# Performance work log

Hardware: AMD Instinct MI355X
Metric: run time of the kernel (lower is better)

Reference implementation:

```python
import jax, jax.numpy as jnp
import numpy as np

SMOOTH = 1e-05
N_SCALES = 3
# 3x3 cross-shaped boundary kernel, OIHW layout [1,1,3,3]
_KERNEL = jnp.array([[0., 1., 0.], [1., 1., 1.], [0., 1., 0.]], jnp.float32).reshape(1, 1, 3, 3)


def _nearest_ds(t, h, w):
    """torch F.interpolate mode='nearest': src_idx = floor(dst_idx * in/out)."""
    H, W = t.shape[-2], t.shape[-1]
    ih = (jnp.arange(h) * H) // h
    iw = (jnp.arange(w) * W) // w
    return t[..., ih[:, None], iw[None, :]]


def _boundary_dou(probs, tgt, valid):
    # probs, tgt: [B,N,h,w] float32; valid: [B,N] float32 in {0,1}
    B, N, h, w = probs.shape
    Y = jax.lax.conv_general_dilated(
        tgt.reshape(B * N, 1, h, w), _KERNEL,
        window_strides=(1, 1), padding=[(1, 1), (1, 1)],
        dimension_numbers=('NCHW', 'OIHW', 'NCHW')).reshape(B, N, h, w)
    Y = Y * tgt
    Y = jnp.where(Y == 5.0, 0.0, Y)  # interior pixels zeroed, boundary kept
    C = jnp.sum(Y != 0, axis=(-2, -1)).astype(jnp.float32)   # [B,N] boundary count
    S = jnp.sum(tgt != 0, axis=(-2, -1)).astype(jnp.float32)  # [B,N] fg count
    alpha = 2.0 * (1.0 - (C + SMOOTH) / (S + SMOOTH)) - 1.0
    alpha = jnp.minimum(alpha, 0.8)
    inter = jnp.sum(probs * tgt, axis=(-2, -1))
    y_sum = jnp.sum(tgt * tgt, axis=(-2, -1))
    z_sum = jnp.sum(probs * probs, axis=(-2, -1))
    dou = (z_sum + y_sum - 2.0 * inter + SMOOTH) / (z_sum + y_sum - (1.0 + alpha) * inter + SMOOTH)
    per = jnp.where(S > 0, dou, probs.mean(axis=(-2, -1)))  # empty-target fallback
    cnt = valid.sum()
    return jnp.where(cnt > 0, (per * valid).sum() / cnt, 0.0)


def reference(logits0, logits1, logits2, targets, valid_mask):
    outs = [logits0, logits1, logits2]
    ws = np.array([1.0 / 2.0 ** i for i in range(N_SCALES)])
    ws = ws / ws.sum()  # nnU-Net deep supervision weights
    tgt_full = targets.astype(jnp.float32)
    valid = (valid_mask >= 0.5).astype(jnp.float32)
    loss = jnp.float32(0.0)
    for w_i, out in zip(ws, outs):
        h, w = out.shape[-2], out.shape[-1]
        tgt = _nearest_ds(tgt_full, h, w)
        probs = jax.nn.sigmoid(out.astype(jnp.float32))
        loss = loss + jnp.float32(w_i) * _boundary_dou(probs, tgt, valid)
    return loss


def setup_inputs() -> dict:
    key = jax.random.key(0)
    k0, k1, k2, kt = jax.random.split(key, 4)
    B, N = 8, 4
    return {
        'logits0': jax.random.normal(k0, (B, N, 512, 512), jnp.float32),
        'logits1': jax.random.normal(k1, (B, N, 256, 256), jnp.float32),
        'logits2': jax.random.normal(k2, (B, N, 128, 128), jnp.float32),
        'targets': jax.random.randint(kt, (B, N, 512, 512), 0, 2, jnp.int32),
        'valid_mask': jnp.ones((B, N), jnp.float32),
    }
```

## Files before the change

kernel.cpp:

```cpp
#include <hip/hip_runtime.h>

#define SMOOTH 1e-5f

typedef float floatx4 __attribute__((ext_vector_type(4)));
typedef float floatx2 __attribute__((ext_vector_type(2)));


__device__ __forceinline__ float wave_reduce(float v) {
#pragma unroll
    for (int off = 32; off; off >>= 1) v += __shfl_down(v, off, 64);
    return v;
}

__device__ __forceinline__ float sigmoidf(float x) {
    return 1.f / (1.f + __expf(-x));
}

__device__ __forceinline__ unsigned pack8(int4 a, int4 b) {
    return (unsigned)(a.x != 0)        | ((unsigned)(a.y != 0) << 1) |
           ((unsigned)(a.z != 0) << 2) | ((unsigned)(a.w != 0) << 3) |
           ((unsigned)(b.x != 0) << 4) | ((unsigned)(b.y != 0) << 5) |
           ((unsigned)(b.z != 0) << 6) | ((unsigned)(b.w != 0) << 7);
}
__device__ __forceinline__ unsigned even4(unsigned b) {
    return (b & 1u) | ((b >> 1) & 2u) | ((b >> 2) & 4u) | ((b >> 3) & 8u);
}
__device__ __forceinline__ unsigned ext2(unsigned b) {
    return (b & 1u) | ((b >> 3) & 2u);
}

template<int W>
__device__ __forceinline__ int stencil_cnt(unsigned u, unsigned c, unsigned d, int lane)
{
    unsigned pv = __shfl_up(c, 1);
    unsigned nx = __shfl_down(c, 1);
    if (lane == 0)  pv = 0;
    if (lane == 63) nx = 0;
    const unsigned M = (1u << W) - 1u;
    unsigned lv = ((c << 1) | ((pv >> (W - 1)) & 1u)) & M;
    unsigned rv = ((c >> 1) | ((nx & 1u) << (W - 1))) & M;
    return __popc(c & ~(u & d & lv & rv));
}

__device__ __forceinline__ void acc_row8(floatx4 a, floatx4 b, unsigned bits,
                                         float& I, float& Z, float& P) {
    float pr[8] = {sigmoidf(a.x), sigmoidf(a.y), sigmoidf(a.z), sigmoidf(a.w),
                   sigmoidf(b.x), sigmoidf(b.y), sigmoidf(b.z), sigmoidf(b.w)};
#pragma unroll
    for (int j = 0; j < 8; ++j) {
        I += ((bits >> j) & 1u) ? pr[j] : 0.f;
        Z += pr[j] * pr[j];
        P += pr[j];
    }
}
__device__ __forceinline__ void acc_row4(floatx4 a, unsigned bits,
                                         float& I, float& Z, float& P) {
    float pr[4] = {sigmoidf(a.x), sigmoidf(a.y), sigmoidf(a.z), sigmoidf(a.w)};
#pragma unroll
    for (int j = 0; j < 4; ++j) {
        I += ((bits >> j) & 1u) ? pr[j] : 0.f;
        Z += pr[j] * pr[j];
        P += pr[j];
    }
}
__device__ __forceinline__ void acc_row2(floatx2 a, unsigned bits,
                                         float& I, float& Z, float& P) {
    float pr[2] = {sigmoidf(a.x), sigmoidf(a.y)};
#pragma unroll
    for (int j = 0; j < 2; ++j) {
        I += ((bits >> j) & 1u) ? pr[j] : 0.f;
        Z += pr[j] * pr[j];
        P += pr[j];
    }
}

__global__ __launch_bounds__(256) void bdou_unified(
    const float* __restrict__ l0, const float* __restrict__ l1,
    const float* __restrict__ l2, const int* __restrict__ tgt,
    float* __restrict__ ws)
{
    const int blk  = blockIdx.x;
    const int tid  = threadIdx.x;
    const int w    = tid >> 6, lane = tid & 63;
    const int img  = blk >> 5;
    const int y0   = (blk & 31) * 16 + w * 4;

    const int*   T  = tgt + (size_t)img * 262144 + lane * 8;
    const float* L0 = l0  + (size_t)img * 262144 + lane * 8;
    const float* L1 = l1  + (size_t)img * 65536  + lane * 4;
    const float* L2 = l2  + (size_t)img * 16384  + lane * 2;

    const int ym4 = (y0 >= 4) ? y0 - 4 : 0;
    const int ym2 = (y0 >= 2) ? y0 - 2 : 0;
    const int ym1 = (y0 >= 1) ? y0 - 1 : 0;
    const int yp4 = (y0 + 4 <= 511) ? y0 + 4 : 511;
    const unsigned mu = (y0 > 0)   ? 0xFFu : 0u;
    const unsigned md = (y0 < 508) ? 0xFFu : 0u;

    int4 tA0 = *(const int4*)(T + (size_t)ym4 * 512), tA1 = *(const int4*)(T + (size_t)ym4 * 512 + 4);
    int4 tB0 = *(const int4*)(T + (size_t)ym2 * 512), tB1 = *(const int4*)(T + (size_t)ym2 * 512 + 4);
    int4 tC0 = *(const int4*)(T + (size_t)ym1 * 512), tC1 = *(const int4*)(T + (size_t)ym1 * 512 + 4);
    int4 t00 = *(const int4*)(T + (size_t)(y0    ) * 512), t01 = *(const int4*)(T + (size_t)(y0    ) * 512 + 4);
    int4 t10 = *(const int4*)(T + (size_t)(y0 + 1) * 512), t11 = *(const int4*)(T + (size_t)(y0 + 1) * 512 + 4);
    int4 t20 = *(const int4*)(T + (size_t)(y0 + 2) * 512), t21 = *(const int4*)(T + (size_t)(y0 + 2) * 512 + 4);
    int4 t30 = *(const int4*)(T + (size_t)(y0 + 3) * 512), t31 = *(const int4*)(T + (size_t)(y0 + 3) * 512 + 4);
    int4 tD0 = *(const int4*)(T + (size_t)yp4 * 512), tD1 = *(const int4*)(T + (size_t)yp4 * 512 + 4);
    floatx4 g00 = *(const floatx4*)(L0 + (size_t)(y0    ) * 512), g01 = *(const floatx4*)(L0 + (size_t)(y0    ) * 512 + 4);
    floatx4 g10 = *(const floatx4*)(L0 + (size_t)(y0 + 1) * 512), g11 = *(const floatx4*)(L0 + (size_t)(y0 + 1) * 512 + 4);
    floatx4 g20 = *(const floatx4*)(L0 + (size_t)(y0 + 2) * 512), g21 = *(const floatx4*)(L0 + (size_t)(y0 + 2) * 512 + 4);
    floatx4 g30 = *(const floatx4*)(L0 + (size_t)(y0 + 3) * 512), g31 = *(const floatx4*)(L0 + (size_t)(y0 + 3) * 512 + 4);
    floatx4 h0  = *(const floatx4*)(L1 + (size_t)(y0 / 2    ) * 256);
    floatx4 h1  = *(const floatx4*)(L1 + (size_t)(y0 / 2 + 1) * 256);
    floatx2 q0  = *(const floatx2*)(L2 + (size_t)(y0 / 4) * 128);

    unsigned bm4 = pack8(tA0, tA1) & mu;
    unsigned bm2 = pack8(tB0, tB1) & mu;
    unsigned bm1 = pack8(tC0, tC1) & mu;
    unsigned b0  = pack8(t00, t01);
    unsigned b1  = pack8(t10, t11);
    unsigned b2  = pack8(t20, t21);
    unsigned b3  = pack8(t30, t31);
    unsigned bp4 = pack8(tD0, tD1) & md;

    int cC0, cS0, cC1, cS1, cC2, cS2;
    float aI0 = 0.f, aZ0 = 0.f, aP0 = 0.f;
    float aI1 = 0.f, aZ1 = 0.f, aP1 = 0.f;
    float aI2 = 0.f, aZ2 = 0.f, aP2 = 0.f;

    cS0 = __popc(b0) + __popc(b1) + __popc(b2) + __popc(b3);
    cC0 = stencil_cnt<8>(bm1, b0, b1, lane) + stencil_cnt<8>(b0, b1, b2, lane) +
          stencil_cnt<8>(b1, b2, b3, lane) + stencil_cnt<8>(b2, b3, bp4, lane);
    acc_row8(g00, g01, b0, aI0, aZ0, aP0);
    acc_row8(g10, g11, b1, aI0, aZ0, aP0);
    acc_row8(g20, g21, b2, aI0, aZ0, aP0);
    acc_row8(g30, g31, b3, aI0, aZ0, aP0);

    {
        unsigned cu = even4(bm2), c0 = even4(b0), c1 = even4(b2), cd = even4(bp4);
        cS1 = __popc(c0) + __popc(c1);
        cC1 = stencil_cnt<4>(cu, c0, c1, lane) + stencil_cnt<4>(c0, c1, cd, lane);
        acc_row4(h0, c0, aI1, aZ1, aP1);
        acc_row4(h1, c1, aI1, aZ1, aP1);
    }

    {
        unsigned zu = ext2(bm4), z = ext2(b0), zd = ext2(bp4);
        cS2 = __popc(z);
        cC2 = stencil_cnt<2>(zu, z, zd, lane);
        acc_row2(q0, z, aI2, aZ2, aP2);
    }

    float vals[15] = {(float)cC0, (float)cS0, aI0, aZ0, aP0,
                      (float)cC1, (float)cS1, aI1, aZ1, aP1,
                      (float)cC2, (float)cS2, aI2, aZ2, aP2};
    __shared__ float red[4][15];
#pragma unroll
    for (int k = 0; k < 15; ++k) vals[k] = wave_reduce(vals[k]);
    if (lane == 0) {
#pragma unroll
        for (int k = 0; k < 15; ++k) red[w][k] = vals[k];
    }
    __syncthreads();
    if (tid < 15) {
        float s = red[0][tid] + red[1][tid] + red[2][tid] + red[3][tid];
        int sc = tid / 5, k = tid - sc * 5;
        atomicAdd(&ws[(sc * 32 + img) * 5 + k], s);
    }
}

__global__ void bdou_final(const float* __restrict__ ws,
                           const float* __restrict__ valid_mask,
                           float* __restrict__ out)
{
    int tid = threadIdx.x;
    float contrib = 0.f, cpart = 0.f;
    if (tid < 96) {
        int s = tid >> 5, i = tid & 31;
        const float* w = ws + tid * 5;
        float C = w[0], S = w[1], I = w[2], Z = w[3], P = w[4];
        float valid = (valid_mask[i] >= 0.5f) ? 1.f : 0.f;
        float alpha = fminf(2.f * (1.f - (C + SMOOTH) / (S + SMOOTH)) - 1.f, 0.8f);
        float dou = (Z + S - 2.f * I + SMOOTH) /
                    (Z + S - (1.f + alpha) * I + SMOOTH);
        const float wts[3]  = {4.f / 7.f, 2.f / 7.f, 1.f / 7.f};
        const float pixc[3] = {262144.f, 65536.f, 16384.f};
        float per = (S > 0.f) ? dou : (P / pixc[s]);
        contrib = wts[s] * per * valid;
        if (tid < 32) cpart = valid;
    }
    contrib = wave_reduce(contrib);
    cpart   = wave_reduce(cpart);
    __shared__ float sm[2][2];
    int wv = tid >> 6, ln = tid & 63;
    if (ln == 0) { sm[wv][0] = contrib; sm[wv][1] = cpart; }
    __syncthreads();
    if (tid == 0) {
        float tot = sm[0][0] + sm[1][0];
        float cnt = sm[0][1] + sm[1][1];
        out[0] = (cnt > 0.f) ? tot / cnt : 0.f;
    }
}

extern "C" void kernel_launch(void* const* d_in, const int* in_sizes, int n_in,
                              void* d_out, int out_size, void* d_ws, size_t ws_size,
                              hipStream_t stream) {
    const float* l0 = (const float*)d_in[0];
    const float* l1 = (const float*)d_in[1];
    const float* l2 = (const float*)d_in[2];
    const int*   tg = (const int*)d_in[3];
    const float* vm = (const float*)d_in[4];
    float* ws = (float*)d_ws;

    (void)hipMemsetAsync(ws, 0, 3 * 32 * 5 * sizeof(float), stream);
    bdou_unified<<<1024, 256, 0, stream>>>(l0, l1, l2, tg, ws);
    bdou_final<<<1, 128, 0, stream>>>(ws, vm, (float*)d_out);
}
```

Baseline: 111.7 us.

## Replace atomic accumulation and memset with per-block slots reduced in final kernel

The main kernel now uses 128-thread blocks covering 8 rows each, launching 2048 blocks. Each block writes its 15 partial sums to its own slot instead of doing global atomicAdds. The final kernel sums the 64 slots per image in parallel with 480 threads. This removes the memset launch and atomic contention, and gives more blocks for load balance. In exchange the final kernel does a serial 64-step strided read.

```diff
diff --git a/kernel.cpp b/kernel.cpp
--- a/kernel.cpp
+++ b/kernel.cpp
@@ -74,16 +74,16 @@
     }
 }
 
-__global__ __launch_bounds__(256) void bdou_unified(
+__global__ __launch_bounds__(128) void bdou_unified(
     const float* __restrict__ l0, const float* __restrict__ l1,
     const float* __restrict__ l2, const int* __restrict__ tgt,
-    float* __restrict__ ws)
+    float* __restrict__ slots)
 {
     const int blk  = blockIdx.x;
     const int tid  = threadIdx.x;
     const int w    = tid >> 6, lane = tid & 63;
-    const int img  = blk >> 5;
-    const int y0   = (blk & 31) * 16 + w * 4;
+    const int img  = blk >> 6;
+    const int y0   = (blk & 63) * 8 + w * 4;
 
     const int*   T  = tgt + (size_t)img * 262144 + lane * 8;
     const float* L0 = l0  + (size_t)img * 262144 + lane * 8;
@@ -153,7 +153,7 @@
     float vals[15] = {(float)cC0, (float)cS0, aI0, aZ0, aP0,
                       (float)cC1, (float)cS1, aI1, aZ1, aP1,
                       (float)cC2, (float)cS2, aI2, aZ2, aP2};
-    __shared__ float red[4][15];
+    __shared__ float red[2][15];
 #pragma unroll
     for (int k = 0; k < 15; ++k) vals[k] = wave_reduce(vals[k]);
     if (lane == 0) {
@@ -161,24 +161,32 @@
         for (int k = 0; k < 15; ++k) red[w][k] = vals[k];
     }
     __syncthreads();
-    if (tid < 15) {
-        float s = red[0][tid] + red[1][tid] + red[2][tid] + red[3][tid];
-        int sc = tid / 5, k = tid - sc * 5;
-        atomicAdd(&ws[(sc * 32 + img) * 5 + k], s);
-    }
-}
-
-__global__ void bdou_final(const float* __restrict__ ws,
-                           const float* __restrict__ valid_mask,
-                           float* __restrict__ out)
+    if (tid < 15) slots[(size_t)blk * 16 + tid] = red[0][tid] + red[1][tid];
+}
+
+__global__ __launch_bounds__(512) void bdou_final(
+    const float* __restrict__ slots, const float* __restrict__ valid_mask,
+    float* __restrict__ out)
 {
-    int tid = threadIdx.x;
+    const int tid = threadIdx.x;
+    __shared__ float sm[480];
+    if (tid < 480) {
+        int cell = tid / 5, k = tid - cell * 5;
+        int s = cell >> 5, img = cell & 31;
+        const float* base = slots + (size_t)img * 64 * 16 + s * 5 + k;
+        float acc = 0.f;
+#pragma unroll 8
+        for (int r = 0; r < 64; ++r) acc += base[r * 16];
+        sm[cell * 5 + k] = acc;
+    }
+    __syncthreads();
+
     float contrib = 0.f, cpart = 0.f;
     if (tid < 96) {
-        int s = tid >> 5, i = tid & 31;
-        const float* w = ws + tid * 5;
-        float C = w[0], S = w[1], I = w[2], Z = w[3], P = w[4];
-        float valid = (valid_mask[i] >= 0.5f) ? 1.f : 0.f;
+        int s = tid >> 5, img = tid & 31;
+        float C = sm[tid * 5 + 0], S = sm[tid * 5 + 1], I = sm[tid * 5 + 2];
+        float Z = sm[tid * 5 + 3], P = sm[tid * 5 + 4];
+        float valid = (valid_mask[img] >= 0.5f) ? 1.f : 0.f;
         float alpha = fminf(2.f * (1.f - (C + SMOOTH) / (S + SMOOTH)) - 1.f, 0.8f);
         float dou = (Z + S - 2.f * I + SMOOTH) /
                     (Z + S - (1.f + alpha) * I + SMOOTH);
@@ -190,13 +198,14 @@
     }
     contrib = wave_reduce(contrib);
     cpart   = wave_reduce(cpart);
-    __shared__ float sm[2][2];
+    __shared__ float r2[8][2];
     int wv = tid >> 6, ln = tid & 63;
-    if (ln == 0) { sm[wv][0] = contrib; sm[wv][1] = cpart; }
+    if (ln == 0) { r2[wv][0] = contrib; r2[wv][1] = cpart; }
     __syncthreads();
     if (tid == 0) {
-        float tot = sm[0][0] + sm[1][0];
-        float cnt = sm[0][1] + sm[1][1];
+        float tot = 0.f, cnt = 0.f;
+#pragma unroll
+        for (int i = 0; i < 8; ++i) { tot += r2[i][0]; cnt += r2[i][1]; }
         out[0] = (cnt > 0.f) ? tot / cnt : 0.f;
     }
 }
@@ -209,9 +218,8 @@
     const float* l2 = (const float*)d_in[2];
     const int*   tg = (const int*)d_in[3];
     const float* vm = (const float*)d_in[4];
-    float* ws = (float*)d_ws;
-
-    (void)hipMemsetAsync(ws, 0, 3 * 32 * 5 * sizeof(float), stream);
-    bdou_unified<<<1024, 256, 0, stream>>>(l0, l1, l2, tg, ws);
-    bdou_final<<<1, 128, 0, stream>>>(ws, vm, (float*)d_out);
-}
+    float* slots = (float*)d_ws;
+
+    bdou_unified<<<2048, 128, 0, stream>>>(l0, l1, l2, tg, slots);
+    bdou_final<<<1, 512, 0, stream>>>(slots, vm, (float*)d_out);
+}
```

Result: slower. 119.0 us (+6.6%).
